# Optimization experiments

Measured on AMD Instinct MI355X. Metric: run time of the kernel, lower is better.

Reference implementation:

```python
import jax, jax.numpy as jnp
import numpy as np

INPUT, HIDDEN, OUTPUT, SEQ = 128, 128, 128, 2048
BATCH = 256

def setup_inputs() -> dict:
    key = jax.random.key(0)
    ks = jax.random.split(key, 6)
    s_x = 1.0 / np.sqrt(INPUT)
    s_h = 1.0 / np.sqrt(HIDDEN)
    return {
        "x": jax.random.normal(ks[0], (BATCH, SEQ, INPUT), jnp.float32),
        "h0": jnp.zeros((BATCH, HIDDEN), jnp.float32),
        # weights stored as [in, out] so forward is x @ W + b (same math as torch Linear)
        "W_xh": jax.random.uniform(ks[1], (INPUT, HIDDEN), jnp.float32, -s_x, s_x),
        "b_xh": jax.random.uniform(ks[2], (HIDDEN,), jnp.float32, -s_x, s_x),
        "W_hh": jax.random.uniform(ks[3], (HIDDEN, HIDDEN), jnp.float32, -s_h, s_h),
        "W_out": jax.random.uniform(ks[4], (HIDDEN, OUTPUT), jnp.float32, -s_h, s_h),
        "b_out": jax.random.uniform(ks[5], (OUTPUT,), jnp.float32, -s_h, s_h),
    }

def reference(x, h0, W_xh, b_xh, W_hh, W_out, b_out):
    # Precompute input projections for all timesteps in one big GEMM: [B,S,H]
    xh = jnp.einsum("bsi,ih->bsh", x, W_xh) + b_xh

    def step(h, xh_t):
        h = jnp.tanh(xh_t + h @ W_hh)
        return h, None

    # scan over time (strict sequential dependency)
    h_last, _ = jax.lax.scan(step, h0, jnp.swapaxes(xh, 0, 1))  # [S,B,H] scan
    # module returns only the last timestep's output projection
    return h_last @ W_out + b_out
```

## Files before the change

### kernel.cpp

```cpp
#include <hip/hip_runtime.h>
#include <hip/hip_bf16.h>


#define SEQ   2048
#define HID   128
#define BATCH 256
#define BD    16

typedef __attribute__((ext_vector_type(8))) short    short8;
typedef __attribute__((ext_vector_type(4))) float    f32x4;
typedef __attribute__((ext_vector_type(4))) float    f4;
typedef __attribute__((ext_vector_type(2))) unsigned u32x2;

union F8 { unsigned u[4]; short8 s; };

__device__ __forceinline__ unsigned pkbf(float a, float b) {
    union { __hip_bfloat16 h[2]; unsigned u; } t;
    t.h[0] = __float2bfloat16(a);
    t.h[1] = __float2bfloat16(b);
    return t.u;
}

__device__ __forceinline__ float blo(unsigned u) {
    union { unsigned v; float f; } t; t.v = u << 16; return t.f;
}
__device__ __forceinline__ float bhi(unsigned u) {
    union { unsigned v; float f; } t; t.v = u & 0xffff0000u; return t.f;
}

__device__ __forceinline__ float tanh_fast(float x) {
    float e = __builtin_amdgcn_exp2f(x * 2.8853900817779268f);
    return 1.0f - 2.0f * __builtin_amdgcn_rcpf(e + 1.0f);
}

__device__ __forceinline__ void block_sync() {
    asm volatile("s_waitcnt lgkmcnt(0)" ::: "memory");
    __builtin_amdgcn_s_barrier();
    asm volatile("" ::: "memory");
}

#define MFMA16(A,B,C) __builtin_amdgcn_mfma_f32_16x16x32_bf16((A),(B),(C),0,0,0)

__launch_bounds__(256, 1)
__global__ void xh_gemm_kernel(const float* __restrict__ x,
                               const float* __restrict__ Wxh,
                               const float* __restrict__ bxh,
                               __hip_bfloat16* __restrict__ xh)
{
    const int tid  = threadIdx.x;
    const int wv   = tid >> 6;
    const int lane = tid & 63;
    const int lg   = lane >> 4;
    const int lm   = lane & 15;

    const int gw = blockIdx.x * 4 + wv;
    const int NW = gridDim.x * 4;
    const int NT = (BATCH * SEQ) / 16;

    short8 wa[8][4];
    {
        #pragma unroll
        for (int T = 0; T < 8; ++T) {
            #pragma unroll
            for (int c = 0; c < 4; ++c) {
                F8 f;
                #pragma unroll
                for (int e2 = 0; e2 < 4; ++e2) {
                    int k = 32*c + 8*lg + 2*e2;
                    f.u[e2] = pkbf(Wxh[(size_t)k*HID + 16*T + lm],
                                   Wxh[(size_t)(k+1)*HID + 16*T + lm]);
                }
                wa[T][c] = f.s;
            }
        }
    }
    float bb[8][4];
    #pragma unroll
    for (int T = 0; T < 8; ++T)
        #pragma unroll
        for (int r = 0; r < 4; ++r)
            bb[T][r] = bxh[16*T + 4*lg + r];

    for (int tile = gw; tile < NT; tile += NW) {
        const float* xp = x + (size_t)tile*16*HID + (size_t)lm*HID + 8*lg;
        f4 s[8];
        #pragma unroll
        for (int c = 0; c < 4; ++c) {
            s[2*c]   = *(const f4*)(xp + 32*c);
            s[2*c+1] = *(const f4*)(xp + 32*c + 4);
        }
        F8 xf[4];
        #pragma unroll
        for (int c = 0; c < 4; ++c) {
            xf[c].u[0] = pkbf(s[2*c][0],   s[2*c][1]);
            xf[c].u[1] = pkbf(s[2*c][2],   s[2*c][3]);
            xf[c].u[2] = pkbf(s[2*c+1][0], s[2*c+1][1]);
            xf[c].u[3] = pkbf(s[2*c+1][2], s[2*c+1][3]);
        }
        __hip_bfloat16* op = xh + (size_t)(tile*16 + lm) * HID;
        #pragma unroll
        for (int T = 0; T < 8; ++T) {
            f32x4 acc = {bb[T][0], bb[T][1], bb[T][2], bb[T][3]};
            #pragma unroll
            for (int c = 0; c < 4; ++c)
                acc = MFMA16(wa[T][c], xf[c].s, acc);
            u32x2 w;
            w[0] = pkbf(acc[0], acc[1]);
            w[1] = pkbf(acc[2], acc[3]);
            *reinterpret_cast<u32x2*>(op + 16*T + 4*lg) = w;
        }
    }
}


#define REC_STEP(SLOT, P, POFF, TRT)                                          \
    {                                                                          \
        f32x4 a0, a1;                                                          \
        a0[0] = blo(SLOT[0][0]); a0[1] = bhi(SLOT[0][0]);                      \
        a0[2] = blo(SLOT[0][1]); a0[3] = bhi(SLOT[0][1]);                      \
        a1[0] = blo(SLOT[1][0]); a1[1] = bhi(SLOT[1][0]);                      \
        a1[2] = blo(SLOT[1][1]); a1[3] = bhi(SLOT[1][1]);                      \
        if ((TRT) + 4 < SEQ) {                                                 \
            SLOT[0] = *(const u32x2*)(xq + (POFF)*256);                        \
            SLOT[1] = *(const u32x2*)(xq + (POFF)*256 + 32);                   \
        }                                                                      \
        block_sync();                              \
        _Pragma("unroll")                                                      \
        for (int c = 0; c < 4; ++c) {                                          \
            short8 hf = *reinterpret_cast<const short8*>(lds + (P)*4096 + rd[c]); \
            a0 = MFMA16(whh[0][c], hf, a0);                                    \
            a1 = MFMA16(whh[1][c], hf, a1);                                    \
        }                                                                      \
        u32x2 w0, w1;                                                          \
        w0[0] = pkbf(tanh_fast(a0[0]), tanh_fast(a0[1]));                      \
        w0[1] = pkbf(tanh_fast(a0[2]), tanh_fast(a0[3]));                      \
        w1[0] = pkbf(tanh_fast(a1[0]), tanh_fast(a1[1]));                      \
        w1[1] = pkbf(tanh_fast(a1[2]), tanh_fast(a1[3]));                      \
        *reinterpret_cast<u32x2*>(lds + ((P)^1)*4096 + hw[0]) = w0;            \
        *reinterpret_cast<u32x2*>(lds + ((P)^1)*4096 + hw[1]) = w1;            \
    }

__launch_bounds__(256, 1)
__global__ void rnn_rec_kernel(const __hip_bfloat16* __restrict__ xh,
                               const float* __restrict__ h0,
                               const float* __restrict__ Whh,
                               const float* __restrict__ Wout,
                               const float* __restrict__ bout,
                               float* __restrict__ out)
{
    __shared__ __align__(16) char lds[2 * 4096];

    const int tid  = threadIdx.x;
    const int wv   = tid >> 6;
    const int lane = tid & 63;
    const int lg   = lane >> 4;
    const int lm   = lane & 15;
    const int b0   = blockIdx.x * BD;

    short8 whh[2][4];
    {
        const int col = 32*wv + lm;
        #pragma unroll
        for (int T = 0; T < 2; ++T) {
            #pragma unroll
            for (int c = 0; c < 4; ++c) {
                F8 f;
                #pragma unroll
                for (int e2 = 0; e2 < 4; ++e2) {
                    int k = 32*c + 8*lg + 2*e2;
                    f.u[e2] = pkbf(Whh[(size_t)k*HID + col + 16*T],
                                   Whh[(size_t)(k+1)*HID + col + 16*T]);
                }
                whh[T][c] = f.s;
            }
        }
    }

    int rd[4];
    #pragma unroll
    for (int c = 0; c < 4; ++c)
        rd[c] = (lm*256 + 64*c + 16*lg) ^ ((lm & 7) << 4);
    int hw[2];
    #pragma unroll
    for (int T = 0; T < 2; ++T)
        hw[T] = (lm*256 + 2*(32*wv + 16*T + 4*lg)) ^ ((lm & 7) << 4);

    {
        int b  = tid >> 4;
        int j0 = (tid & 15) * 8;
        const float* hp = h0 + (size_t)(b0 + b) * HID + j0;
        f4 v0 = *(const f4*)(hp);
        f4 v1 = *(const f4*)(hp + 4);
        F8 f;
        f.u[0] = pkbf(v0[0], v0[1]); f.u[1] = pkbf(v0[2], v0[3]);
        f.u[2] = pkbf(v1[0], v1[1]); f.u[3] = pkbf(v1[2], v1[3]);
        int off = (b*256 + 2*j0) ^ ((b & 7) << 4);
        *reinterpret_cast<short8*>(lds + off) = f.s;
    }

    const char* xq = (const char*)xh
                   + ((size_t)(b0 + lm) * SEQ) * (HID*2)
                   + (size_t)(32*wv + 4*lg) * 2;

    u32x2 pA[2], pB[2], pC[2], pD[2];
    pA[0] = *(const u32x2*)(xq + 0*256);      pA[1] = *(const u32x2*)(xq + 0*256 + 32);
    pB[0] = *(const u32x2*)(xq + 1*256);      pB[1] = *(const u32x2*)(xq + 1*256 + 32);
    pC[0] = *(const u32x2*)(xq + 2*256);      pC[1] = *(const u32x2*)(xq + 2*256 + 32);
    pD[0] = *(const u32x2*)(xq + 3*256);      pD[1] = *(const u32x2*)(xq + 3*256 + 32);

    for (int t = 0; t < SEQ; t += 4) {
        REC_STEP(pA, 0, 4, t);
        REC_STEP(pB, 1, 5, t + 1);
        REC_STEP(pC, 0, 6, t + 2);
        REC_STEP(pD, 1, 7, t + 3);
        xq += 4 * 256;
    }

    block_sync();
    {
        short8 wo[2][4];
        const int col = 32*wv + lm;
        #pragma unroll
        for (int T = 0; T < 2; ++T) {
            #pragma unroll
            for (int c = 0; c < 4; ++c) {
                F8 f;
                #pragma unroll
                for (int e2 = 0; e2 < 4; ++e2) {
                    int k = 32*c + 8*lg + 2*e2;
                    f.u[e2] = pkbf(Wout[(size_t)k*HID + col + 16*T],
                                   Wout[(size_t)(k+1)*HID + col + 16*T]);
                }
                wo[T][c] = f.s;
            }
        }
        f32x4 o0 = {bout[32*wv + 4*lg + 0], bout[32*wv + 4*lg + 1],
                    bout[32*wv + 4*lg + 2], bout[32*wv + 4*lg + 3]};
        f32x4 o1 = {bout[32*wv + 16 + 4*lg + 0], bout[32*wv + 16 + 4*lg + 1],
                    bout[32*wv + 16 + 4*lg + 2], bout[32*wv + 16 + 4*lg + 3]};
        #pragma unroll
        for (int c = 0; c < 4; ++c) {
            short8 hf = *reinterpret_cast<const short8*>(lds + rd[c]);
            o0 = MFMA16(wo[0][c], hf, o0);
            o1 = MFMA16(wo[1][c], hf, o1);
        }
        float* op = out + (size_t)(b0 + lm) * HID + 32*wv + 4*lg;
        *reinterpret_cast<f4*>(op)      = o0;
        *reinterpret_cast<f4*>(op + 16) = o1;
    }
}

#define RNN_STEP(SLOT, P, POFF, TRT)                                          \
    {                                                                          \
        F8 xf[4];                                                              \
        _Pragma("unroll")                                                      \
        for (int c = 0; c < 4; ++c) {                                          \
            xf[c].u[0] = pkbf(SLOT[2*c][0],   SLOT[2*c][1]);                   \
            xf[c].u[1] = pkbf(SLOT[2*c][2],   SLOT[2*c][3]);                   \
            xf[c].u[2] = pkbf(SLOT[2*c+1][0], SLOT[2*c+1][1]);                 \
            xf[c].u[3] = pkbf(SLOT[2*c+1][2], SLOT[2*c+1][3]);                 \
        }                                                                      \
        if ((TRT) + 2 < SEQ) {                                                 \
            _Pragma("unroll")                                                  \
            for (int c = 0; c < 4; ++c) {                                      \
                SLOT[2*c]   = *(const f4*)(xq + (POFF)*HID + 32*c);            \
                SLOT[2*c+1] = *(const f4*)(xq + (POFF)*HID + 32*c + 4);        \
            }                                                                  \
        }                                                                      \
        f32x4 a0 = {bx[0][0], bx[0][1], bx[0][2], bx[0][3]};                   \
        f32x4 a1 = {bx[1][0], bx[1][1], bx[1][2], bx[1][3]};                   \
        _Pragma("unroll")                                                      \
        for (int c = 0; c < 4; ++c) {                                          \
            a0 = MFMA16(wxh[0][c], xf[c].s, a0);                               \
            a1 = MFMA16(wxh[1][c], xf[c].s, a1);                               \
        }                                                                      \
        block_sync();                                                          \
        _Pragma("unroll")                                                      \
        for (int c = 0; c < 4; ++c) {                                          \
            short8 hf = *reinterpret_cast<const short8*>(lds + (P)*4096 + rd[c]); \
            a0 = MFMA16(whh[0][c], hf, a0);                                    \
            a1 = MFMA16(whh[1][c], hf, a1);                                    \
        }                                                                      \
        u32x2 w0, w1;                                                          \
        w0[0] = pkbf(tanh_fast(a0[0]), tanh_fast(a0[1]));                      \
        w0[1] = pkbf(tanh_fast(a0[2]), tanh_fast(a0[3]));                      \
        w1[0] = pkbf(tanh_fast(a1[0]), tanh_fast(a1[1]));                      \
        w1[1] = pkbf(tanh_fast(a1[2]), tanh_fast(a1[3]));                      \
        *reinterpret_cast<u32x2*>(lds + ((P)^1)*4096 + hw[0]) = w0;            \
        *reinterpret_cast<u32x2*>(lds + ((P)^1)*4096 + hw[1]) = w1;            \
    }

__launch_bounds__(256, 1)
__global__ void rnn_fused_kernel(const float* __restrict__ x,
                                 const float* __restrict__ h0,
                                 const float* __restrict__ Wxh,
                                 const float* __restrict__ bxh,
                                 const float* __restrict__ Whh,
                                 const float* __restrict__ Wout,
                                 const float* __restrict__ bout,
                                 float* __restrict__ out)
{
    __shared__ __align__(16) char lds[2 * 4096];

    const int tid  = threadIdx.x;
    const int wv   = tid >> 6;
    const int lane = tid & 63;
    const int lg   = lane >> 4;
    const int lm   = lane & 15;
    const int b0   = blockIdx.x * BD;

    short8 wxh[2][4], whh[2][4];
    {
        const int col = 32*wv + lm;
        #pragma unroll
        for (int T = 0; T < 2; ++T) {
            #pragma unroll
            for (int c = 0; c < 4; ++c) {
                F8 fx, fh;
                #pragma unroll
                for (int e2 = 0; e2 < 4; ++e2) {
                    int k = 32*c + 8*lg + 2*e2;
                    fx.u[e2] = pkbf(Wxh[(size_t)k*HID + col + 16*T],
                                    Wxh[(size_t)(k+1)*HID + col + 16*T]);
                    fh.u[e2] = pkbf(Whh[(size_t)k*HID + col + 16*T],
                                    Whh[(size_t)(k+1)*HID + col + 16*T]);
                }
                wxh[T][c] = fx.s; whh[T][c] = fh.s;
            }
        }
    }
    float bx[2][4];
    #pragma unroll
    for (int T = 0; T < 2; ++T)
        #pragma unroll
        for (int r = 0; r < 4; ++r)
            bx[T][r] = bxh[32*wv + 16*T + 4*lg + r];

    int rd[4];
    #pragma unroll
    for (int c = 0; c < 4; ++c)
        rd[c] = (lm*256 + 64*c + 16*lg) ^ ((lm & 7) << 4);
    int hw[2];
    #pragma unroll
    for (int T = 0; T < 2; ++T)
        hw[T] = (lm*256 + 2*(32*wv + 16*T + 4*lg)) ^ ((lm & 7) << 4);

    {
        int b  = tid >> 4;
        int j0 = (tid & 15) * 8;
        const float* hp = h0 + (size_t)(b0 + b) * HID + j0;
        f4 v0 = *(const f4*)(hp);
        f4 v1 = *(const f4*)(hp + 4);
        F8 f;
        f.u[0] = pkbf(v0[0], v0[1]); f.u[1] = pkbf(v0[2], v0[3]);
        f.u[2] = pkbf(v1[0], v1[1]); f.u[3] = pkbf(v1[2], v1[3]);
        int off = (b*256 + 2*j0) ^ ((b & 7) << 4);
        *reinterpret_cast<short8*>(lds + off) = f.s;
    }

    const float* xq = x + (size_t)(b0 + lm) * SEQ * HID + 8*lg;
    f4 sA[8], sB[8];
    #pragma unroll
    for (int c = 0; c < 4; ++c) {
        sA[2*c]   = *(const f4*)(xq + 32*c);
        sA[2*c+1] = *(const f4*)(xq + 32*c + 4);
        sB[2*c]   = *(const f4*)(xq + HID + 32*c);
        sB[2*c+1] = *(const f4*)(xq + HID + 32*c + 4);
    }

    for (int t = 0; t < SEQ; t += 2) {
        RNN_STEP(sA, 0, 2, t);
        RNN_STEP(sB, 1, 3, t + 1);
        xq += 2 * HID;
    }

    block_sync();
    {
        short8 wo[2][4];
        const int col = 32*wv + lm;
        #pragma unroll
        for (int T = 0; T < 2; ++T) {
            #pragma unroll
            for (int c = 0; c < 4; ++c) {
                F8 f;
                #pragma unroll
                for (int e2 = 0; e2 < 4; ++e2) {
                    int k = 32*c + 8*lg + 2*e2;
                    f.u[e2] = pkbf(Wout[(size_t)k*HID + col + 16*T],
                                   Wout[(size_t)(k+1)*HID + col + 16*T]);
                }
                wo[T][c] = f.s;
            }
        }
        f32x4 o0 = {bout[32*wv + 4*lg + 0], bout[32*wv + 4*lg + 1],
                    bout[32*wv + 4*lg + 2], bout[32*wv + 4*lg + 3]};
        f32x4 o1 = {bout[32*wv + 16 + 4*lg + 0], bout[32*wv + 16 + 4*lg + 1],
                    bout[32*wv + 16 + 4*lg + 2], bout[32*wv + 16 + 4*lg + 3]};
        #pragma unroll
        for (int c = 0; c < 4; ++c) {
            short8 hf = *reinterpret_cast<const short8*>(lds + rd[c]);
            o0 = MFMA16(wo[0][c], hf, o0);
            o1 = MFMA16(wo[1][c], hf, o1);
        }
        float* op = out + (size_t)(b0 + lm) * HID + 32*wv + 4*lg;
        *reinterpret_cast<f4*>(op)      = o0;
        *reinterpret_cast<f4*>(op + 16) = o1;
    }
}

extern "C" void kernel_launch(void* const* d_in, const int* in_sizes, int n_in,
                              void* d_out, int out_size, void* d_ws, size_t ws_size,
                              hipStream_t stream) {
    const float* x    = (const float*)d_in[0];
    const float* h0   = (const float*)d_in[1];
    const float* Wxh  = (const float*)d_in[2];
    const float* bxh  = (const float*)d_in[3];
    const float* Whh  = (const float*)d_in[4];
    const float* Wout = (const float*)d_in[5];
    const float* bout = (const float*)d_in[6];
    (void)in_sizes; (void)n_in; (void)out_size;

    const size_t need = (size_t)BATCH * SEQ * HID * 2;
    if (ws_size >= need) {
        __hip_bfloat16* xh = (__hip_bfloat16*)d_ws;
        xh_gemm_kernel<<<dim3(512), dim3(256), 0, stream>>>(x, Wxh, bxh, xh);
        rnn_rec_kernel<<<dim3(BATCH / BD), dim3(256), 0, stream>>>(
            xh, h0, Whh, Wout, bout, (float*)d_out);
    } else {
        rnn_fused_kernel<<<dim3(BATCH / BD), dim3(256), 0, stream>>>(
            x, h0, Wxh, bxh, Whh, Wout, bout, (float*)d_out);
    }
}
```

Measured before the change: 1.032 ms.

## Keep each wave's own hidden fragment in registers and use fragment-linear LDS layout

Permutes the W_hh columns each wave owns so that its MFMA output lines up directly with the B-operand fragment layout. Each wave now keeps its own slice of h in registers and reads only the other three fragments from LDS. The LDS buffer switches from a swizzled row layout to a linear per-fragment layout, written with one 16-byte store. The x projection is fetched with one 16-byte load instead of two 8-byte loads. The self-fragment MFMA is issued before the LDS reads complete, and the work is split across two accumulator chains to shorten the serial per-step latency. The cost is more intricate index mapping that must stay consistent with the xh layout and the final projection.

Result: slower. 1.057 ms (+2.5%).

```diff
diff --git a/kernel.cpp b/kernel.cpp
--- a/kernel.cpp
+++ b/kernel.cpp
@@ -11,6 +11,7 @@
 typedef __attribute__((ext_vector_type(4))) float    f32x4;
 typedef __attribute__((ext_vector_type(4))) float    f4;
 typedef __attribute__((ext_vector_type(2))) unsigned u32x2;
+typedef __attribute__((ext_vector_type(4))) unsigned u32x4;
 
 union F8 { unsigned u[4]; short8 s; };
 
@@ -116,28 +117,34 @@
 #define REC_STEP(SLOT, P, POFF, TRT)                                          \
     {                                                                          \
         f32x4 a0, a1;                                                          \
-        a0[0] = blo(SLOT[0][0]); a0[1] = bhi(SLOT[0][0]);                      \
-        a0[2] = blo(SLOT[0][1]); a0[3] = bhi(SLOT[0][1]);                      \
-        a1[0] = blo(SLOT[1][0]); a1[1] = bhi(SLOT[1][0]);                      \
-        a1[2] = blo(SLOT[1][1]); a1[3] = bhi(SLOT[1][1]);                      \
-        if ((TRT) + 4 < SEQ) {                                                 \
-            SLOT[0] = *(const u32x2*)(xq + (POFF)*256);                        \
-            SLOT[1] = *(const u32x2*)(xq + (POFF)*256 + 32);                   \
-        }                                                                      \
-        block_sync();                              \
-        _Pragma("unroll")                                                      \
-        for (int c = 0; c < 4; ++c) {                                          \
-            short8 hf = *reinterpret_cast<const short8*>(lds + (P)*4096 + rd[c]); \
-            a0 = MFMA16(whh[0][c], hf, a0);                                    \
-            a1 = MFMA16(whh[1][c], hf, a1);                                    \
-        }                                                                      \
-        u32x2 w0, w1;                                                          \
-        w0[0] = pkbf(tanh_fast(a0[0]), tanh_fast(a0[1]));                      \
-        w0[1] = pkbf(tanh_fast(a0[2]), tanh_fast(a0[3]));                      \
-        w1[0] = pkbf(tanh_fast(a1[0]), tanh_fast(a1[1]));                      \
-        w1[1] = pkbf(tanh_fast(a1[2]), tanh_fast(a1[3]));                      \
-        *reinterpret_cast<u32x2*>(lds + ((P)^1)*4096 + hw[0]) = w0;            \
-        *reinterpret_cast<u32x2*>(lds + ((P)^1)*4096 + hw[1]) = w1;            \
+        a0[0] = blo(SLOT[0]); a0[1] = bhi(SLOT[0]);                            \
+        a0[2] = blo(SLOT[1]); a0[3] = bhi(SLOT[1]);                            \
+        a1[0] = blo(SLOT[2]); a1[1] = bhi(SLOT[2]);                            \
+        a1[2] = blo(SLOT[3]); a1[3] = bhi(SLOT[3]);                            \
+        if ((TRT) + 4 < SEQ) SLOT = *(const u32x4*)(xq + (POFF)*256);          \
+        block_sync();                         \
+        const char* rb = lds + (P)*4096;                                       \
+        short8 fA = *(const short8*)(rb + rdA);                                \
+        short8 fB = *(const short8*)(rb + rdB);                                \
+        short8 fC = *(const short8*)(rb + rdC);                                \
+        f32x4 t0 = {0.f,0.f,0.f,0.f}, t1 = {0.f,0.f,0.f,0.f};                  \
+               \
+        a0 = MFMA16(whhf[0][3], selffrag, a0);                                 \
+        a1 = MFMA16(whhf[1][3], selffrag, a1);                                 \
+        t0 = MFMA16(whhf[0][0], fA, t0);                                       \
+        t1 = MFMA16(whhf[1][0], fA, t1);                                       \
+        a0 = MFMA16(whhf[0][1], fB, a0);                                       \
+        a1 = MFMA16(whhf[1][1], fB, a1);                                       \
+        t0 = MFMA16(whhf[0][2], fC, t0);                                       \
+        t1 = MFMA16(whhf[1][2], fC, t1);                                       \
+        a0 += t0; a1 += t1;                                                    \
+        F8 nf;                                                                 \
+        nf.u[0] = pkbf(tanh_fast(a0[0]), tanh_fast(a0[1]));                    \
+        nf.u[1] = pkbf(tanh_fast(a0[2]), tanh_fast(a0[3]));                    \
+        nf.u[2] = pkbf(tanh_fast(a1[0]), tanh_fast(a1[1]));                    \
+        nf.u[3] = pkbf(tanh_fast(a1[2]), tanh_fast(a1[3]));                    \
+        selffrag = nf.s;                                                       \
+        *reinterpret_cast<short8*>(lds + ((P)^1)*4096 + wrO) = selffrag;       \
     }
 
 __launch_bounds__(256, 1)
@@ -157,68 +164,64 @@
     const int lm   = lane & 15;
     const int b0   = blockIdx.x * BD;
 
-    short8 whh[2][4];
-    {
-        const int col = 32*wv + lm;
-        #pragma unroll
-        for (int T = 0; T < 2; ++T) {
-            #pragma unroll
-            for (int c = 0; c < 4; ++c) {
+    const int cA = (wv + 1) & 3, cB = (wv + 2) & 3, cC = (wv + 3) & 3;
+    short8 whhf[2][4];
+    {
+        const int scol = 32*wv + 8*(lm >> 2) + (lm & 3);
+        const int cs[4] = {cA, cB, cC, wv};
+        #pragma unroll
+        for (int u = 0; u < 2; ++u) {
+            #pragma unroll
+            for (int ci = 0; ci < 4; ++ci) {
+                const int c = cs[ci];
                 F8 f;
                 #pragma unroll
                 for (int e2 = 0; e2 < 4; ++e2) {
                     int k = 32*c + 8*lg + 2*e2;
-                    f.u[e2] = pkbf(Whh[(size_t)k*HID + col + 16*T],
-                                   Whh[(size_t)(k+1)*HID + col + 16*T]);
+                    f.u[e2] = pkbf(Whh[(size_t)k*HID + scol + 4*u],
+                                   Whh[(size_t)(k+1)*HID + scol + 4*u]);
                 }
-                whh[T][c] = f.s;
+                whhf[u][ci] = f.s;
             }
         }
     }
 
-    int rd[4];
-    #pragma unroll
-    for (int c = 0; c < 4; ++c)
-        rd[c] = (lm*256 + 64*c + 16*lg) ^ ((lm & 7) << 4);
-    int hw[2];
-    #pragma unroll
-    for (int T = 0; T < 2; ++T)
-        hw[T] = (lm*256 + 2*(32*wv + 16*T + 4*lg)) ^ ((lm & 7) << 4);
-
-    {
-        int b  = tid >> 4;
-        int j0 = (tid & 15) * 8;
-        const float* hp = h0 + (size_t)(b0 + b) * HID + j0;
+    const int rdA = cA*1024 + lane*16;
+    const int rdB = cB*1024 + lane*16;
+    const int rdC = cC*1024 + lane*16;
+    const int wrO = wv*1024 + lane*16;
+
+    short8 selffrag;
+    {
+        const float* hp = h0 + (size_t)(b0 + lm) * HID + 32*wv + 8*lg;
         f4 v0 = *(const f4*)(hp);
         f4 v1 = *(const f4*)(hp + 4);
         F8 f;
         f.u[0] = pkbf(v0[0], v0[1]); f.u[1] = pkbf(v0[2], v0[3]);
         f.u[2] = pkbf(v1[0], v1[1]); f.u[3] = pkbf(v1[2], v1[3]);
-        int off = (b*256 + 2*j0) ^ ((b & 7) << 4);
-        *reinterpret_cast<short8*>(lds + off) = f.s;
-    }
-
-    const char* xq = (const char*)xh
-                   + ((size_t)(b0 + lm) * SEQ) * (HID*2)
-                   + (size_t)(32*wv + 4*lg) * 2;
-
-    u32x2 pA[2], pB[2], pC[2], pD[2];
-    pA[0] = *(const u32x2*)(xq + 0*256);      pA[1] = *(const u32x2*)(xq + 0*256 + 32);
-    pB[0] = *(const u32x2*)(xq + 1*256);      pB[1] = *(const u32x2*)(xq + 1*256 + 32);
-    pC[0] = *(const u32x2*)(xq + 2*256);      pC[1] = *(const u32x2*)(xq + 2*256 + 32);
-    pD[0] = *(const u32x2*)(xq + 3*256);      pD[1] = *(const u32x2*)(xq + 3*256 + 32);
+        selffrag = f.s;
+        *reinterpret_cast<short8*>(lds + wrO) = selffrag;
+    }
+
+    const char* xq = (const char*)xh + (size_t)(b0 + lm) * SEQ * 256
+                   + 64*wv + 16*lg;
+
+    u32x4 sA = *(const u32x4*)(xq + 0*256);
+    u32x4 sB = *(const u32x4*)(xq + 1*256);
+    u32x4 sC = *(const u32x4*)(xq + 2*256);
+    u32x4 sD = *(const u32x4*)(xq + 3*256);
 
     for (int t = 0; t < SEQ; t += 4) {
-        REC_STEP(pA, 0, 4, t);
-        REC_STEP(pB, 1, 5, t + 1);
-        REC_STEP(pC, 0, 6, t + 2);
-        REC_STEP(pD, 1, 7, t + 3);
+        REC_STEP(sA, 0, 4, t);
+        REC_STEP(sB, 1, 5, t + 1);
+        REC_STEP(sC, 0, 6, t + 2);
+        REC_STEP(sD, 1, 7, t + 3);
         xq += 4 * 256;
     }
 
     block_sync();
     {
-        short8 wo[2][4];
+        short8 wof[2][4];
         const int col = 32*wv + lm;
         #pragma unroll
         for (int T = 0; T < 2; ++T) {
@@ -231,7 +234,7 @@
                     f.u[e2] = pkbf(Wout[(size_t)k*HID + col + 16*T],
                                    Wout[(size_t)(k+1)*HID + col + 16*T]);
                 }
-                wo[T][c] = f.s;
+                wof[T][c] = f.s;
             }
         }
         f32x4 o0 = {bout[32*wv + 4*lg + 0], bout[32*wv + 4*lg + 1],
@@ -240,9 +243,9 @@
                     bout[32*wv + 16 + 4*lg + 2], bout[32*wv + 16 + 4*lg + 3]};
         #pragma unroll
         for (int c = 0; c < 4; ++c) {
-            short8 hf = *reinterpret_cast<const short8*>(lds + rd[c]);
-            o0 = MFMA16(wo[0][c], hf, o0);
-            o1 = MFMA16(wo[1][c], hf, o1);
+            short8 hf = *reinterpret_cast<const short8*>(lds + c*1024 + lane*16);
+            o0 = MFMA16(wof[0][c], hf, o0);
+            o1 = MFMA16(wof[1][c], hf, o1);
         }
         float* op = out + (size_t)(b0 + lm) * HID + 32*wv + 4*lg;
         *reinterpret_cast<f4*>(op)      = o0;
```

## Run recurrence in a single wavefront with register-resident hidden state

Applied to the files above, without the earlier changes.

The recurrence kernel moves from four wavefronts that exchange the hidden state through LDS with a block barrier every step to one wavefront per 16-row batch tile. That wavefront issues all 32 MFMAs per step. W_hh columns are permuted so each accumulator's output layout matches the B-operand layout needed for the next step, which lets h stay in registers with no LDS traffic or barrier. The cost is four times more serial MFMA work per wave and only 16 waves in total, so per-step latency could rise even though the synchronisation is gone.

Measured after the change: 1.848 ms. 1.79x slower.

```diff
diff --git a/kernel.cpp b/kernel.cpp
--- a/kernel.cpp
+++ b/kernel.cpp
@@ -11,6 +11,7 @@
 typedef __attribute__((ext_vector_type(4))) float    f32x4;
 typedef __attribute__((ext_vector_type(4))) float    f4;
 typedef __attribute__((ext_vector_type(2))) unsigned u32x2;
+typedef __attribute__((ext_vector_type(4))) unsigned u32x4;
 
 union F8 { unsigned u[4]; short8 s; };
 
@@ -113,140 +114,120 @@
 }
 
 
-#define REC_STEP(SLOT, P, POFF, TRT)                                          \
+#define REC1W_STEP(S, POFF, TRT)                                              \
     {                                                                          \
-        f32x4 a0, a1;                                                          \
-        a0[0] = blo(SLOT[0][0]); a0[1] = bhi(SLOT[0][0]);                      \
-        a0[2] = blo(SLOT[0][1]); a0[3] = bhi(SLOT[0][1]);                      \
-        a1[0] = blo(SLOT[1][0]); a1[1] = bhi(SLOT[1][0]);                      \
-        a1[2] = blo(SLOT[1][1]); a1[3] = bhi(SLOT[1][1]);                      \
+        f32x4 acc[8];                                                          \
+        _Pragma("unroll")                                                      \
+        for (int c = 0; c < 4; ++c) {                                          \
+            acc[c][0]   = blo(S[c][0]); acc[c][1]   = bhi(S[c][0]);            \
+            acc[c][2]   = blo(S[c][1]); acc[c][3]   = bhi(S[c][1]);            \
+            acc[c+4][0] = blo(S[c][2]); acc[c+4][1] = bhi(S[c][2]);            \
+            acc[c+4][2] = blo(S[c][3]); acc[c+4][3] = bhi(S[c][3]);            \
+        }                                                                      \
         if ((TRT) + 4 < SEQ) {                                                 \
-            SLOT[0] = *(const u32x2*)(xq + (POFF)*256);                        \
-            SLOT[1] = *(const u32x2*)(xq + (POFF)*256 + 32);                   \
-        }                                                                      \
-        block_sync();                              \
-        _Pragma("unroll")                                                      \
-        for (int c = 0; c < 4; ++c) {                                          \
-            short8 hf = *reinterpret_cast<const short8*>(lds + (P)*4096 + rd[c]); \
-            a0 = MFMA16(whh[0][c], hf, a0);                                    \
-            a1 = MFMA16(whh[1][c], hf, a1);                                    \
-        }                                                                      \
-        u32x2 w0, w1;                                                          \
-        w0[0] = pkbf(tanh_fast(a0[0]), tanh_fast(a0[1]));                      \
-        w0[1] = pkbf(tanh_fast(a0[2]), tanh_fast(a0[3]));                      \
-        w1[0] = pkbf(tanh_fast(a1[0]), tanh_fast(a1[1]));                      \
-        w1[1] = pkbf(tanh_fast(a1[2]), tanh_fast(a1[3]));                      \
-        *reinterpret_cast<u32x2*>(lds + ((P)^1)*4096 + hw[0]) = w0;            \
-        *reinterpret_cast<u32x2*>(lds + ((P)^1)*4096 + hw[1]) = w1;            \
-    }
-
-__launch_bounds__(256, 1)
-__global__ void rnn_rec_kernel(const __hip_bfloat16* __restrict__ xh,
-                               const float* __restrict__ h0,
-                               const float* __restrict__ Whh,
-                               const float* __restrict__ Wout,
-                               const float* __restrict__ bout,
-                               float* __restrict__ out)
+            _Pragma("unroll")                                                  \
+            for (int c = 0; c < 4; ++c)                                        \
+                S[c] = *(const u32x4*)(xq + (POFF)*256 + 64*c);                \
+        }                                                                      \
+        _Pragma("unroll")                                                      \
+        for (int c = 0; c < 4; ++c) {                                          \
+            _Pragma("unroll")                                                  \
+            for (int T = 0; T < 8; ++T)                                        \
+                acc[T] = MFMA16(whf[T][c], hb[c], acc[T]);                     \
+        }                                                                      \
+        _Pragma("unroll")                                                      \
+        for (int c = 0; c < 4; ++c) {                                          \
+            F8 nf;                                                             \
+            nf.u[0] = pkbf(tanh_fast(acc[c][0]),   tanh_fast(acc[c][1]));      \
+            nf.u[1] = pkbf(tanh_fast(acc[c][2]),   tanh_fast(acc[c][3]));      \
+            nf.u[2] = pkbf(tanh_fast(acc[c+4][0]), tanh_fast(acc[c+4][1]));    \
+            nf.u[3] = pkbf(tanh_fast(acc[c+4][2]), tanh_fast(acc[c+4][3]));    \
+            hb[c] = nf.s;                                                      \
+        }                                                                      \
+    }
+
+__launch_bounds__(64, 1)
+__global__ void rnn_rec1w_kernel(const __hip_bfloat16* __restrict__ xh,
+                                 const float* __restrict__ h0,
+                                 const float* __restrict__ Whh,
+                                 const float* __restrict__ Wout,
+                                 const float* __restrict__ bout,
+                                 float* __restrict__ out)
 {
-    __shared__ __align__(16) char lds[2 * 4096];
-
-    const int tid  = threadIdx.x;
-    const int wv   = tid >> 6;
-    const int lane = tid & 63;
+    const int lane = threadIdx.x & 63;
     const int lg   = lane >> 4;
     const int lm   = lane & 15;
     const int b0   = blockIdx.x * BD;
 
-    short8 whh[2][4];
-    {
-        const int col = 32*wv + lm;
-        #pragma unroll
-        for (int T = 0; T < 2; ++T) {
+    short8 whf[8][4];
+    {
+        #pragma unroll
+        for (int T = 0; T < 8; ++T) {
+            const int jcol = 32*(T & 3) + 8*(lm >> 2) + 4*(T >> 2) + (lm & 3);
             #pragma unroll
             for (int c = 0; c < 4; ++c) {
                 F8 f;
                 #pragma unroll
                 for (int e2 = 0; e2 < 4; ++e2) {
                     int k = 32*c + 8*lg + 2*e2;
-                    f.u[e2] = pkbf(Whh[(size_t)k*HID + col + 16*T],
-                                   Whh[(size_t)(k+1)*HID + col + 16*T]);
+                    f.u[e2] = pkbf(Whh[(size_t)k*HID + jcol],
+                                   Whh[(size_t)(k+1)*HID + jcol]);
                 }
-                whh[T][c] = f.s;
+                whf[T][c] = f.s;
             }
         }
     }
 
-    int rd[4];
-    #pragma unroll
-    for (int c = 0; c < 4; ++c)
-        rd[c] = (lm*256 + 64*c + 16*lg) ^ ((lm & 7) << 4);
-    int hw[2];
-    #pragma unroll
-    for (int T = 0; T < 2; ++T)
-        hw[T] = (lm*256 + 2*(32*wv + 16*T + 4*lg)) ^ ((lm & 7) << 4);
-
-    {
-        int b  = tid >> 4;
-        int j0 = (tid & 15) * 8;
-        const float* hp = h0 + (size_t)(b0 + b) * HID + j0;
+    short8 hb[4];
+    #pragma unroll
+    for (int c = 0; c < 4; ++c) {
+        const float* hp = h0 + (size_t)(b0 + lm) * HID + 32*c + 8*lg;
         f4 v0 = *(const f4*)(hp);
         f4 v1 = *(const f4*)(hp + 4);
         F8 f;
         f.u[0] = pkbf(v0[0], v0[1]); f.u[1] = pkbf(v0[2], v0[3]);
         f.u[2] = pkbf(v1[0], v1[1]); f.u[3] = pkbf(v1[2], v1[3]);
-        int off = (b*256 + 2*j0) ^ ((b & 7) << 4);
-        *reinterpret_cast<short8*>(lds + off) = f.s;
-    }
-
-    const char* xq = (const char*)xh
-                   + ((size_t)(b0 + lm) * SEQ) * (HID*2)
-                   + (size_t)(32*wv + 4*lg) * 2;
-
-    u32x2 pA[2], pB[2], pC[2], pD[2];
-    pA[0] = *(const u32x2*)(xq + 0*256);      pA[1] = *(const u32x2*)(xq + 0*256 + 32);
-    pB[0] = *(const u32x2*)(xq + 1*256);      pB[1] = *(const u32x2*)(xq + 1*256 + 32);
-    pC[0] = *(const u32x2*)(xq + 2*256);      pC[1] = *(const u32x2*)(xq + 2*256 + 32);
-    pD[0] = *(const u32x2*)(xq + 3*256);      pD[1] = *(const u32x2*)(xq + 3*256 + 32);
+        hb[c] = f.s;
+    }
+
+    const char* xq = (const char*)xh + (size_t)(b0 + lm) * SEQ * 256 + 16*lg;
+
+    u32x4 SA[4], SB[4], SC[4], SD[4];
+    #pragma unroll
+    for (int c = 0; c < 4; ++c) {
+        SA[c] = *(const u32x4*)(xq + 0*256 + 64*c);
+        SB[c] = *(const u32x4*)(xq + 1*256 + 64*c);
+        SC[c] = *(const u32x4*)(xq + 2*256 + 64*c);
+        SD[c] = *(const u32x4*)(xq + 3*256 + 64*c);
+    }
 
     for (int t = 0; t < SEQ; t += 4) {
-        REC_STEP(pA, 0, 4, t);
-        REC_STEP(pB, 1, 5, t + 1);
-        REC_STEP(pC, 0, 6, t + 2);
-        REC_STEP(pD, 1, 7, t + 3);
+        REC1W_STEP(SA, 4, t);
+        REC1W_STEP(SB, 5, t + 1);
+        REC1W_STEP(SC, 6, t + 2);
+        REC1W_STEP(SD, 7, t + 3);
         xq += 4 * 256;
     }
 
-    block_sync();
-    {
-        short8 wo[2][4];
-        const int col = 32*wv + lm;
-        #pragma unroll
-        for (int T = 0; T < 2; ++T) {
+    {
+        #pragma unroll
+        for (int T = 0; T < 8; ++T) {
+            f32x4 o = {bout[16*T + 4*lg + 0], bout[16*T + 4*lg + 1],
+                       bout[16*T + 4*lg + 2], bout[16*T + 4*lg + 3]};
             #pragma unroll
             for (int c = 0; c < 4; ++c) {
                 F8 f;
                 #pragma unroll
                 for (int e2 = 0; e2 < 4; ++e2) {
                     int k = 32*c + 8*lg + 2*e2;
-                    f.u[e2] = pkbf(Wout[(size_t)k*HID + col + 16*T],
-                                   Wout[(size_t)(k+1)*HID + col + 16*T]);
+                    f.u[e2] = pkbf(Wout[(size_t)k*HID + 16*T + lm],
+                                   Wout[(size_t)(k+1)*HID + 16*T + lm]);
                 }
-                wo[T][c] = f.s;
+                o = MFMA16(f.s, hb[c], o);
             }
-        }
-        f32x4 o0 = {bout[32*wv + 4*lg + 0], bout[32*wv + 4*lg + 1],
-                    bout[32*wv + 4*lg + 2], bout[32*wv + 4*lg + 3]};
-        f32x4 o1 = {bout[32*wv + 16 + 4*lg + 0], bout[32*wv + 16 + 4*lg + 1],
-                    bout[32*wv + 16 + 4*lg + 2], bout[32*wv + 16 + 4*lg + 3]};
-        #pragma unroll
-        for (int c = 0; c < 4; ++c) {
-            short8 hf = *reinterpret_cast<const short8*>(lds + rd[c]);
-            o0 = MFMA16(wo[0][c], hf, o0);
-            o1 = MFMA16(wo[1][c], hf, o1);
-        }
-        float* op = out + (size_t)(b0 + lm) * HID + 32*wv + 4*lg;
-        *reinterpret_cast<f4*>(op)      = o0;
-        *reinterpret_cast<f4*>(op + 16) = o1;
+            float* op = out + (size_t)(b0 + lm) * HID + 16*T + 4*lg;
+            *reinterpret_cast<f4*>(op) = o;
+        }
     }
 }
 
@@ -424,7 +405,7 @@
     if (ws_size >= need) {
         __hip_bfloat16* xh = (__hip_bfloat16*)d_ws;
         xh_gemm_kernel<<<dim3(512), dim3(256), 0, stream>>>(x, Wxh, bxh, xh);
-        rnn_rec_kernel<<<dim3(BATCH / BD), dim3(256), 0, stream>>>(
+        rnn_rec1w_kernel<<<dim3(BATCH / BD), dim3(64), 0, stream>>>(
             xh, h0, Whh, Wout, bout, (float*)d_out);
     } else {
         rnn_fused_kernel<<<dim3(BATCH / BD), dim3(256), 0, stream>>>(
```
